# Kernel tuning notes

Measured on AMD Instinct MI355X. Metric: run time of the kernel, lower is better.

## Reference

```python
import jax, jax.numpy as jnp
import numpy as np

E = 8        # num_experts
TOP_K = 2    # num_experts_per_tok
H = 2048     # hidden_size
I = 1408     # moe_intermediate_size

def setup_inputs() -> dict:
    key = jax.random.key(0)
    k0, k1, k2, k3, k4 = jax.random.split(key, 5)
    hidden_states = jax.random.normal(k0, (2, 2048, H), dtype=jnp.float32)
    gate_w = jax.random.normal(k1, (E, H), dtype=jnp.float32) * 0.02   # router: Linear(H, E)
    wg = jax.random.normal(k2, (E, I, H), dtype=jnp.float32) * 0.02    # gate_proj per expert
    wu = jax.random.normal(k3, (E, I, H), dtype=jnp.float32) * 0.02    # up_proj per expert
    wd = jax.random.normal(k4, (E, H, I), dtype=jnp.float32) * 0.02    # down_proj per expert
    return {"hidden_states": hidden_states, "gate_w": gate_w, "wg": wg, "wu": wu, "wd": wd}

def reference(hidden_states, gate_w, wg, wu, wd):
    b, s, h = hidden_states.shape
    x = hidden_states.reshape(-1, h)                      # [T, H]
    router_logits = x @ gate_w.T                          # [T, E]
    routing_weights = jax.nn.softmax(router_logits.astype(jnp.float32), axis=-1)
    topk_weight, topk_idx = jax.lax.top_k(routing_weights, TOP_K)   # [T, K]
    topk_weight = topk_weight / jnp.sum(topk_weight, axis=-1, keepdims=True)
    # per-token combine weight for each expert: w[t,e] = sum_k topk_weight[t,k] * [topk_idx[t,k]==e]
    comb = jnp.sum(jax.nn.one_hot(topk_idx, E, dtype=x.dtype) * topk_weight[..., None].astype(x.dtype), axis=1)  # [T, E]
    # compute each expert on all tokens (dense faithful equivalent of masked dispatch), combine with comb
    def expert_out(e):
        g = x @ wg[e].T                                   # [T, I]
        u = x @ wu[e].T                                   # [T, I]
        return (jax.nn.silu(g) * u) @ wd[e].T             # [T, H]
    y = jnp.zeros_like(x)
    for e in range(E):  # small fixed expert count
        y = y + expert_out(e) * comb[:, e:e+1]
    final = y.reshape(b, s, h)
    return final, router_logits.astype(hidden_states.dtype)
```

## Files before the change

### kernel.cpp

```cpp
#include <hip/hip_runtime.h>

#define NTOK 4096
#define NEXP 8
#define HD 2048
#define ID 1408

typedef unsigned short u16;
typedef __attribute__((ext_vector_type(8))) short short8;
typedef __attribute__((ext_vector_type(4))) float f32x4;
typedef const __attribute__((address_space(1))) void* gas_ptr;
typedef __attribute__((address_space(3))) void* las_ptr;

__device__ __forceinline__ u16 f2bf(float f) {
  unsigned int u = __float_as_uint(f);
  u += 0x7FFFu + ((u >> 16) & 1u);
  return (u16)(u >> 16);
}

__device__ __forceinline__ void async16(const u16* g, u16* l) {
  __builtin_amdgcn_global_load_lds((gas_ptr)g, (las_ptr)l, 16, 0, 0);
}

__global__ void cvt_kernel(const float* __restrict__ s, u16* __restrict__ d, long n8) {
  long i = (long)blockIdx.x * blockDim.x + threadIdx.x;
  if (i >= n8) return;
  const float4* s4 = (const float4*)s;
  float4 a = s4[2*i], b = s4[2*i+1];
  short8 o;
  o[0] = (short)f2bf(a.x); o[1] = (short)f2bf(a.y);
  o[2] = (short)f2bf(a.z); o[3] = (short)f2bf(a.w);
  o[4] = (short)f2bf(b.x); o[5] = (short)f2bf(b.y);
  o[6] = (short)f2bf(b.z); o[7] = (short)f2bf(b.w);
  *(short8*)(d + 8*i) = o;
}

__global__ void router_kernel(const float* __restrict__ x, const float* __restrict__ gw,
                              float* __restrict__ logits, int* __restrict__ cnt,
                              int* __restrict__ ptok, float* __restrict__ pw) {
  int t = blockIdx.x * 4 + (threadIdx.x >> 6);
  int lane = threadIdx.x & 63;
  if (t >= NTOK) return;
  const float4* xr = (const float4*)(x + (size_t)t * HD);
  float dot[NEXP];
#pragma unroll
  for (int e = 0; e < NEXP; ++e) dot[e] = 0.f;
#pragma unroll
  for (int c = 0; c < 8; ++c) {
    float4 xv = xr[c*64 + lane];
#pragma unroll
    for (int e = 0; e < NEXP; ++e) {
      float4 gv = ((const float4*)(gw + e*HD))[c*64 + lane];
      dot[e] += xv.x*gv.x + xv.y*gv.y + xv.z*gv.z + xv.w*gv.w;
    }
  }
#pragma unroll
  for (int off = 32; off > 0; off >>= 1) {
#pragma unroll
    for (int e = 0; e < NEXP; ++e) dot[e] += __shfl_xor(dot[e], off);
  }
  if (lane < NEXP) logits[(size_t)t*NEXP + lane] = dot[lane];
  if (lane == 0) {
    float mx = dot[0];
#pragma unroll
    for (int e = 1; e < NEXP; ++e) mx = fmaxf(mx, dot[e]);
    float p[NEXP];
#pragma unroll
    for (int e = 0; e < NEXP; ++e) p[e] = __expf(dot[e] - mx);
    int e0 = 0;
#pragma unroll
    for (int e = 1; e < NEXP; ++e) if (p[e] > p[e0]) e0 = e;
    int e1 = (e0 == 0) ? 1 : 0;
#pragma unroll
    for (int e = 0; e < NEXP; ++e) if (e != e0 && p[e] > p[e1]) e1 = e;
    float denom = p[e0] + p[e1];
    int pos0 = atomicAdd(&cnt[e0], 1);
    ptok[e0*NTOK + pos0] = t; pw[e0*NTOK + pos0] = p[e0] / denom;
    int pos1 = atomicAdd(&cnt[e1], 1);
    ptok[e1*NTOK + pos1] = t; pw[e1*NTOK + pos1] = p[e1] / denom;
  }
}

__global__ void prefix_kernel(const int* __restrict__ cnt, int* __restrict__ offs) {
  if (threadIdx.x == 0) {
    int a = 0;
    for (int e = 0; e < NEXP; ++e) { offs[e] = a; a += cnt[e]; }
  }
}

__global__ __launch_bounds__(256, 2) void gemm1_kernel(
    const u16* __restrict__ xb, const u16* __restrict__ wgb, const u16* __restrict__ wub,
    const int* __restrict__ cnt, const int* __restrict__ offs,
    const int* __restrict__ ptok, u16* __restrict__ hbuf) {
  int e = blockIdx.z, mt = blockIdx.y, nt = blockIdx.x;
  int c = cnt[e];
  if (mt * 128 >= c) return;
  int off = offs[e];

  __shared__ u16 sA[128*32], sBg[128*32], sBu[128*32];

  int tid = threadIdx.x;
  int r0 = tid >> 2;
  int ch = (tid & 3) * 8;
  int s0 = mt*128 + r0, s1 = s0 + 64;
  int t0 = ptok[e*NTOK + (s0 < c ? s0 : 0)];
  int t1 = ptok[e*NTOK + (s1 < c ? s1 : 0)];
  const u16* ga0 = xb + (size_t)t0*HD + ch;
  const u16* ga1 = xb + (size_t)t1*HD + ch;
  int n0 = nt*128 + r0;
  const u16* gg0 = wgb + ((size_t)e*ID + n0)*HD + ch;
  const u16* gg1 = gg0 + (size_t)64*HD;
  const u16* gu0 = wub + ((size_t)e*ID + n0)*HD + ch;
  const u16* gu1 = gu0 + (size_t)64*HD;

  int lane = tid & 63, wv = tid >> 6, wr = wv >> 1, wc = wv & 1;
  int fm = lane & 15, kg = lane >> 4;

  f32x4 accg[4][4], accu[4][4];
#pragma unroll
  for (int i = 0; i < 4; ++i)
#pragma unroll
    for (int j = 0; j < 4; ++j) {
      accg[i][j] = {0.f, 0.f, 0.f, 0.f};
      accu[i][j] = {0.f, 0.f, 0.f, 0.f};
    }

  const u16* sAf  = sA  + (wr*64 + fm)*32 + kg*8;
  const u16* sBgf = sBg + (wc*64 + fm)*32 + kg*8;
  const u16* sBuf = sBu + (wc*64 + fm)*32 + kg*8;

  for (int k0 = 0; k0 < HD; k0 += 32) {
    async16(ga0 + k0, sA + tid*8);
    async16(ga1 + k0, sA + 2048 + tid*8);
    async16(gg0 + k0, sBg + tid*8);
    async16(gg1 + k0, sBg + 2048 + tid*8);
    async16(gu0 + k0, sBu + tid*8);
    async16(gu1 + k0, sBu + 2048 + tid*8);
    __syncthreads();
    short8 af[4], bg[4], bu[4];
#pragma unroll
    for (int i = 0; i < 4; ++i) af[i] = *(const short8*)(sAf + i*512);
#pragma unroll
    for (int j = 0; j < 4; ++j) {
      bg[j] = *(const short8*)(sBgf + j*512);
      bu[j] = *(const short8*)(sBuf + j*512);
    }
#pragma unroll
    for (int i = 0; i < 4; ++i)
#pragma unroll
      for (int j = 0; j < 4; ++j) {
        accg[i][j] = __builtin_amdgcn_mfma_f32_16x16x32_bf16(af[i], bg[j], accg[i][j], 0, 0, 0);
        accu[i][j] = __builtin_amdgcn_mfma_f32_16x16x32_bf16(af[i], bu[j], accu[i][j], 0, 0, 0);
      }
    __syncthreads();
  }

#pragma unroll
  for (int i = 0; i < 4; ++i) {
#pragma unroll
    for (int r = 0; r < 4; ++r) {
      int slot = mt*128 + wr*64 + i*16 + kg*4 + r;
      if (slot < c) {
        size_t rowb = (size_t)(off + slot) * ID + nt*128 + wc*64 + fm;
#pragma unroll
        for (int j = 0; j < 4; ++j) {
          float g = accg[i][j][r], u = accu[i][j][r];
          float hh = g * u / (1.f + __expf(-g));
          hbuf[rowb + (size_t)j*16] = f2bf(hh);
        }
      }
    }
  }
}

__global__ __launch_bounds__(256, 2) void gemm2_kernel(
    const u16* __restrict__ hbuf, const u16* __restrict__ wdb,
    const int* __restrict__ cnt, const int* __restrict__ offs,
    const int* __restrict__ ptok, const float* __restrict__ pw,
    float* __restrict__ out) {
  int e = blockIdx.z, mt = blockIdx.y, nt = blockIdx.x;
  int c = cnt[e];
  if (mt * 128 >= c) return;
  int off = offs[e];

  __shared__ u16 sA[128*32], sB[128*32];

  int tid = threadIdx.x;
  int r0 = tid >> 2;
  int ch = (tid & 3) * 8;
  int s0 = mt*128 + r0, s1 = s0 + 64;
  const u16* ga0 = hbuf + (size_t)(off + (s0 < c ? s0 : 0))*ID + ch;
  const u16* ga1 = hbuf + (size_t)(off + (s1 < c ? s1 : 0))*ID + ch;
  int n0 = nt*128 + r0;
  const u16* gb0 = wdb + ((size_t)e*HD + n0)*ID + ch;
  const u16* gb1 = gb0 + (size_t)64*ID;

  int lane = tid & 63, wv = tid >> 6, wr = wv >> 1, wc = wv & 1;
  int fm = lane & 15, kg = lane >> 4;

  f32x4 acc[4][4];
#pragma unroll
  for (int i = 0; i < 4; ++i)
#pragma unroll
    for (int j = 0; j < 4; ++j) acc[i][j] = {0.f, 0.f, 0.f, 0.f};

  const u16* sAf = sA + (wr*64 + fm)*32 + kg*8;
  const u16* sBf = sB + (wc*64 + fm)*32 + kg*8;

  for (int k0 = 0; k0 < ID; k0 += 32) {
    async16(ga0 + k0, sA + tid*8);
    async16(ga1 + k0, sA + 2048 + tid*8);
    async16(gb0 + k0, sB + tid*8);
    async16(gb1 + k0, sB + 2048 + tid*8);
    __syncthreads();
    short8 af[4], bf[4];
#pragma unroll
    for (int i = 0; i < 4; ++i) af[i] = *(const short8*)(sAf + i*512);
#pragma unroll
    for (int j = 0; j < 4; ++j) bf[j] = *(const short8*)(sBf + j*512);
#pragma unroll
    for (int i = 0; i < 4; ++i)
#pragma unroll
      for (int j = 0; j < 4; ++j)
        acc[i][j] = __builtin_amdgcn_mfma_f32_16x16x32_bf16(af[i], bf[j], acc[i][j], 0, 0, 0);
    __syncthreads();
  }

#pragma unroll
  for (int i = 0; i < 4; ++i) {
#pragma unroll
    for (int r = 0; r < 4; ++r) {
      int slot = mt*128 + wr*64 + i*16 + kg*4 + r;
      if (slot < c) {
        int tok = ptok[e*NTOK + slot];
        float wgt = pw[e*NTOK + slot];
        float* orow = out + (size_t)tok*HD + nt*128 + wc*64 + fm;
#pragma unroll
        for (int j = 0; j < 4; ++j)
          atomicAdd(orow + j*16, wgt * acc[i][j][r]);
      }
    }
  }
}

extern "C" void kernel_launch(void* const* d_in, const int* in_sizes, int n_in,
                              void* d_out, int out_size, void* d_ws, size_t ws_size,
                              hipStream_t stream) {
  const float* x  = (const float*)d_in[0];
  const float* gw = (const float*)d_in[1];
  const float* wg = (const float*)d_in[2];
  const float* wu = (const float*)d_in[3];
  const float* wd = (const float*)d_in[4];
  float* out = (float*)d_out;

  char* p = (char*)d_ws;
  u16*   xb   = (u16*)(p);
  u16*   wgb  = (u16*)(p + 16777216UL);
  u16*   wub  = (u16*)(p + 62914560UL);
  u16*   wdb  = (u16*)(p + 109051904UL);
  u16*   hbuf = (u16*)(p + 155189248UL);
  int*   ptok = (int*)(p + 178257920UL);
  float* pww  = (float*)(p + 178388992UL);
  int*   cnt  = (int*)(p + 178520064UL);
  int*   offs = (int*)(p + 178520320UL);

  hipMemsetAsync(out, 0, (size_t)NTOK * HD * sizeof(float), stream);
  hipMemsetAsync(cnt, 0, NEXP * sizeof(int), stream);

  cvt_kernel<<<4096, 256, 0, stream>>>(x, xb, (long)NTOK * HD / 8);
  cvt_kernel<<<11264, 256, 0, stream>>>(wg, wgb, (long)NEXP * ID * HD / 8);
  cvt_kernel<<<11264, 256, 0, stream>>>(wu, wub, (long)NEXP * ID * HD / 8);
  cvt_kernel<<<11264, 256, 0, stream>>>(wd, wdb, (long)NEXP * HD * ID / 8);

  router_kernel<<<1024, 256, 0, stream>>>(x, gw, out + (size_t)NTOK * HD, cnt, ptok, pww);
  prefix_kernel<<<1, 64, 0, stream>>>(cnt, offs);

  gemm1_kernel<<<dim3(11, 32, 8), 256, 0, stream>>>(xb, wgb, wub, cnt, offs, ptok, hbuf);
  gemm2_kernel<<<dim3(16, 32, 8), 256, 0, stream>>>(hbuf, wdb, cnt, offs, ptok, pww, out);
}
```

Measured before the change: 699.8 us.

## Drop LDS staging in GEMMs, fuse x conversion into router, replace atomics with combine

Both GEMM kernels now load MFMA fragments straight from global memory into registers, removing the LDS staging and the two barriers per k-step. The x-to-bf16 conversion moves into the router kernel, which saves a launch and one pass over x. Routing entries now carry a rank bit, so gemm2 writes weighted bf16 per-rank outputs into a scratch buffer without atomics, and a new combine kernel sums the two ranks into the fp32 output, which also removes the output memset. The risks are uncoalesced global fragment loads with no shared reuse across waves, extra rounding from storing the expert outputs in bf16, and ybuf aliasing xb, which is only safe because xb is dead by the time gemm2 runs.

```diff
diff --git a/kernel.cpp b/kernel.cpp
--- a/kernel.cpp
+++ b/kernel.cpp
@@ -7,18 +7,16 @@
 
 typedef unsigned short u16;
 typedef __attribute__((ext_vector_type(8))) short short8;
+typedef __attribute__((ext_vector_type(4))) unsigned short ushort4v;
 typedef __attribute__((ext_vector_type(4))) float f32x4;
-typedef const __attribute__((address_space(1))) void* gas_ptr;
-typedef __attribute__((address_space(3))) void* las_ptr;
 
 __device__ __forceinline__ u16 f2bf(float f) {
   unsigned int u = __float_as_uint(f);
   u += 0x7FFFu + ((u >> 16) & 1u);
   return (u16)(u >> 16);
 }
-
-__device__ __forceinline__ void async16(const u16* g, u16* l) {
-  __builtin_amdgcn_global_load_lds((gas_ptr)g, (las_ptr)l, 16, 0, 0);
+__device__ __forceinline__ float bf2f(u16 b) {
+  return __uint_as_float(((unsigned int)b) << 16);
 }
 
 __global__ void cvt_kernel(const float* __restrict__ s, u16* __restrict__ d, long n8) {
@@ -35,6 +33,7 @@
 }
 
 __global__ void router_kernel(const float* __restrict__ x, const float* __restrict__ gw,
+                              u16* __restrict__ xb,
                               float* __restrict__ logits, int* __restrict__ cnt,
                               int* __restrict__ ptok, float* __restrict__ pw) {
   int t = blockIdx.x * 4 + (threadIdx.x >> 6);
@@ -47,6 +46,9 @@
 #pragma unroll
   for (int c = 0; c < 8; ++c) {
     float4 xv = xr[c*64 + lane];
+    ushort4v o;
+    o[0] = f2bf(xv.x); o[1] = f2bf(xv.y); o[2] = f2bf(xv.z); o[3] = f2bf(xv.w);
+    *(ushort4v*)(xb + (size_t)t*HD + (c*64 + lane)*4) = o;
 #pragma unroll
     for (int e = 0; e < NEXP; ++e) {
       float4 gv = ((const float4*)(gw + e*HD))[c*64 + lane];
@@ -74,9 +76,11 @@
     for (int e = 0; e < NEXP; ++e) if (e != e0 && p[e] > p[e1]) e1 = e;
     float denom = p[e0] + p[e1];
     int pos0 = atomicAdd(&cnt[e0], 1);
-    ptok[e0*NTOK + pos0] = t; pw[e0*NTOK + pos0] = p[e0] / denom;
+    ptok[e0*NTOK + pos0] = t;
+    pw[e0*NTOK + pos0] = p[e0] / denom;
     int pos1 = atomicAdd(&cnt[e1], 1);
-    ptok[e1*NTOK + pos1] = t; pw[e1*NTOK + pos1] = p[e1] / denom;
+    ptok[e1*NTOK + pos1] = t | 0x10000;
+    pw[e1*NTOK + pos1] = p[e1] / denom;
   }
 }
 
@@ -96,24 +100,26 @@
   if (mt * 128 >= c) return;
   int off = offs[e];
 
-  __shared__ u16 sA[128*32], sBg[128*32], sBu[128*32];
-
   int tid = threadIdx.x;
-  int r0 = tid >> 2;
-  int ch = (tid & 3) * 8;
-  int s0 = mt*128 + r0, s1 = s0 + 64;
-  int t0 = ptok[e*NTOK + (s0 < c ? s0 : 0)];
-  int t1 = ptok[e*NTOK + (s1 < c ? s1 : 0)];
-  const u16* ga0 = xb + (size_t)t0*HD + ch;
-  const u16* ga1 = xb + (size_t)t1*HD + ch;
-  int n0 = nt*128 + r0;
-  const u16* gg0 = wgb + ((size_t)e*ID + n0)*HD + ch;
-  const u16* gg1 = gg0 + (size_t)64*HD;
-  const u16* gu0 = wub + ((size_t)e*ID + n0)*HD + ch;
-  const u16* gu1 = gu0 + (size_t)64*HD;
-
   int lane = tid & 63, wv = tid >> 6, wr = wv >> 1, wc = wv & 1;
   int fm = lane & 15, kg = lane >> 4;
+
+  const u16* aptr[4];
+#pragma unroll
+  for (int i = 0; i < 4; ++i) {
+    int m = mt*128 + wr*64 + i*16 + fm;
+    int mm = m < c ? m : c - 1;
+    int tok = ptok[e*NTOK + mm] & 0xFFFF;
+    aptr[i] = xb + (size_t)tok*HD + kg*8;
+  }
+  const u16* gptr[4];
+  const u16* uptr[4];
+#pragma unroll
+  for (int j = 0; j < 4; ++j) {
+    int n = nt*128 + wc*64 + j*16 + fm;
+    gptr[j] = wgb + ((size_t)e*ID + n)*HD + kg*8;
+    uptr[j] = wub + ((size_t)e*ID + n)*HD + kg*8;
+  }
 
   f32x4 accg[4][4], accu[4][4];
 #pragma unroll
@@ -124,25 +130,14 @@
       accu[i][j] = {0.f, 0.f, 0.f, 0.f};
     }
 
-  const u16* sAf  = sA  + (wr*64 + fm)*32 + kg*8;
-  const u16* sBgf = sBg + (wc*64 + fm)*32 + kg*8;
-  const u16* sBuf = sBu + (wc*64 + fm)*32 + kg*8;
-
   for (int k0 = 0; k0 < HD; k0 += 32) {
-    async16(ga0 + k0, sA + tid*8);
-    async16(ga1 + k0, sA + 2048 + tid*8);
-    async16(gg0 + k0, sBg + tid*8);
-    async16(gg1 + k0, sBg + 2048 + tid*8);
-    async16(gu0 + k0, sBu + tid*8);
-    async16(gu1 + k0, sBu + 2048 + tid*8);
-    __syncthreads();
     short8 af[4], bg[4], bu[4];
 #pragma unroll
-    for (int i = 0; i < 4; ++i) af[i] = *(const short8*)(sAf + i*512);
+    for (int i = 0; i < 4; ++i) af[i] = *(const short8*)(aptr[i] + k0);
 #pragma unroll
     for (int j = 0; j < 4; ++j) {
-      bg[j] = *(const short8*)(sBgf + j*512);
-      bu[j] = *(const short8*)(sBuf + j*512);
+      bg[j] = *(const short8*)(gptr[j] + k0);
+      bu[j] = *(const short8*)(uptr[j] + k0);
     }
 #pragma unroll
     for (int i = 0; i < 4; ++i)
@@ -151,7 +146,6 @@
         accg[i][j] = __builtin_amdgcn_mfma_f32_16x16x32_bf16(af[i], bg[j], accg[i][j], 0, 0, 0);
         accu[i][j] = __builtin_amdgcn_mfma_f32_16x16x32_bf16(af[i], bu[j], accu[i][j], 0, 0, 0);
       }
-    __syncthreads();
   }
 
 #pragma unroll
@@ -176,53 +170,48 @@
     const u16* __restrict__ hbuf, const u16* __restrict__ wdb,
     const int* __restrict__ cnt, const int* __restrict__ offs,
     const int* __restrict__ ptok, const float* __restrict__ pw,
-    float* __restrict__ out) {
+    u16* __restrict__ ybuf) {
   int e = blockIdx.z, mt = blockIdx.y, nt = blockIdx.x;
   int c = cnt[e];
   if (mt * 128 >= c) return;
   int off = offs[e];
 
-  __shared__ u16 sA[128*32], sB[128*32];
-
   int tid = threadIdx.x;
-  int r0 = tid >> 2;
-  int ch = (tid & 3) * 8;
-  int s0 = mt*128 + r0, s1 = s0 + 64;
-  const u16* ga0 = hbuf + (size_t)(off + (s0 < c ? s0 : 0))*ID + ch;
-  const u16* ga1 = hbuf + (size_t)(off + (s1 < c ? s1 : 0))*ID + ch;
-  int n0 = nt*128 + r0;
-  const u16* gb0 = wdb + ((size_t)e*HD + n0)*ID + ch;
-  const u16* gb1 = gb0 + (size_t)64*ID;
-
   int lane = tid & 63, wv = tid >> 6, wr = wv >> 1, wc = wv & 1;
   int fm = lane & 15, kg = lane >> 4;
 
+  const u16* aptr[4];
+#pragma unroll
+  for (int i = 0; i < 4; ++i) {
+    int m = mt*128 + wr*64 + i*16 + fm;
+    int mm = m < c ? m : c - 1;
+    aptr[i] = hbuf + (size_t)(off + mm)*ID + kg*8;
+  }
+  const u16* bptr[4];
+#pragma unroll
+  for (int j = 0; j < 4; ++j) {
+    int n = nt*128 + wc*64 + j*16 + fm;
+    bptr[j] = wdb + ((size_t)e*HD + n)*ID + kg*8;
+  }
+
   f32x4 acc[4][4];
 #pragma unroll
   for (int i = 0; i < 4; ++i)
 #pragma unroll
     for (int j = 0; j < 4; ++j) acc[i][j] = {0.f, 0.f, 0.f, 0.f};
 
-  const u16* sAf = sA + (wr*64 + fm)*32 + kg*8;
-  const u16* sBf = sB + (wc*64 + fm)*32 + kg*8;
-
+#pragma unroll 2
   for (int k0 = 0; k0 < ID; k0 += 32) {
-    async16(ga0 + k0, sA + tid*8);
-    async16(ga1 + k0, sA + 2048 + tid*8);
-    async16(gb0 + k0, sB + tid*8);
-    async16(gb1 + k0, sB + 2048 + tid*8);
-    __syncthreads();
     short8 af[4], bf[4];
 #pragma unroll
-    for (int i = 0; i < 4; ++i) af[i] = *(const short8*)(sAf + i*512);
-#pragma unroll
-    for (int j = 0; j < 4; ++j) bf[j] = *(const short8*)(sBf + j*512);
+    for (int i = 0; i < 4; ++i) af[i] = *(const short8*)(aptr[i] + k0);
+#pragma unroll
+    for (int j = 0; j < 4; ++j) bf[j] = *(const short8*)(bptr[j] + k0);
 #pragma unroll
     for (int i = 0; i < 4; ++i)
 #pragma unroll
       for (int j = 0; j < 4; ++j)
         acc[i][j] = __builtin_amdgcn_mfma_f32_16x16x32_bf16(af[i], bf[j], acc[i][j], 0, 0, 0);
-    __syncthreads();
   }
 
 #pragma unroll
@@ -231,15 +220,36 @@
     for (int r = 0; r < 4; ++r) {
       int slot = mt*128 + wr*64 + i*16 + kg*4 + r;
       if (slot < c) {
-        int tok = ptok[e*NTOK + slot];
+        int entry = ptok[e*NTOK + slot];
+        int tok = entry & 0xFFFF;
+        int rank = entry >> 16;
         float wgt = pw[e*NTOK + slot];
-        float* orow = out + (size_t)tok*HD + nt*128 + wc*64 + fm;
+        u16* orow = ybuf + ((size_t)tok*2 + rank)*HD + nt*128 + wc*64 + fm;
 #pragma unroll
         for (int j = 0; j < 4; ++j)
-          atomicAdd(orow + j*16, wgt * acc[i][j][r]);
+          orow[j*16] = f2bf(wgt * acc[i][j][r]);
       }
     }
   }
+}
+
+__global__ void combine_kernel(const u16* __restrict__ ybuf, float* __restrict__ out) {
+  int t = blockIdx.x;
+  int col = threadIdx.x * 8;
+  short8 a = *(const short8*)(ybuf + ((size_t)t*2)*HD + col);
+  short8 b = *(const short8*)(ybuf + ((size_t)t*2 + 1)*HD + col);
+  float4 o0, o1;
+  o0.x = bf2f((u16)a[0]) + bf2f((u16)b[0]);
+  o0.y = bf2f((u16)a[1]) + bf2f((u16)b[1]);
+  o0.z = bf2f((u16)a[2]) + bf2f((u16)b[2]);
+  o0.w = bf2f((u16)a[3]) + bf2f((u16)b[3]);
+  o1.x = bf2f((u16)a[4]) + bf2f((u16)b[4]);
+  o1.y = bf2f((u16)a[5]) + bf2f((u16)b[5]);
+  o1.z = bf2f((u16)a[6]) + bf2f((u16)b[6]);
+  o1.w = bf2f((u16)a[7]) + bf2f((u16)b[7]);
+  float4* dst = (float4*)(out + (size_t)t*HD + col);
+  dst[0] = o0;
+  dst[1] = o1;
 }
 
 extern "C" void kernel_launch(void* const* d_in, const int* in_sizes, int n_in,
@@ -253,6 +263,7 @@
   float* out = (float*)d_out;
 
   char* p = (char*)d_ws;
+  u16*   ybuf = (u16*)(p);
   u16*   xb   = (u16*)(p);
   u16*   wgb  = (u16*)(p + 16777216UL);
   u16*   wub  = (u16*)(p + 62914560UL);
@@ -263,17 +274,16 @@
   int*   cnt  = (int*)(p + 178520064UL);
   int*   offs = (int*)(p + 178520320UL);
 
-  hipMemsetAsync(out, 0, (size_t)NTOK * HD * sizeof(float), stream);
   hipMemsetAsync(cnt, 0, NEXP * sizeof(int), stream);
 
-  cvt_kernel<<<4096, 256, 0, stream>>>(x, xb, (long)NTOK * HD / 8);
   cvt_kernel<<<11264, 256, 0, stream>>>(wg, wgb, (long)NEXP * ID * HD / 8);
   cvt_kernel<<<11264, 256, 0, stream>>>(wu, wub, (long)NEXP * ID * HD / 8);
   cvt_kernel<<<11264, 256, 0, stream>>>(wd, wdb, (long)NEXP * HD * ID / 8);
 
-  router_kernel<<<1024, 256, 0, stream>>>(x, gw, out + (size_t)NTOK * HD, cnt, ptok, pww);
+  router_kernel<<<1024, 256, 0, stream>>>(x, gw, xb, out + (size_t)NTOK * HD, cnt, ptok, pww);
   prefix_kernel<<<1, 64, 0, stream>>>(cnt, offs);
 
   gemm1_kernel<<<dim3(11, 32, 8), 256, 0, stream>>>(xb, wgb, wub, cnt, offs, ptok, hbuf);
-  gemm2_kernel<<<dim3(16, 32, 8), 256, 0, stream>>>(hbuf, wdb, cnt, offs, ptok, pww, out);
-}
+  gemm2_kernel<<<dim3(16, 32, 8), 256, 0, stream>>>(hbuf, wdb, cnt, offs, ptok, pww, ybuf);
+  combine_kernel<<<NTOK, 256, 0, stream>>>(ybuf, out);
+}
```

After: 1.012 ms. 44.7% more time.
